# Performance work log

Hardware: AMD Instinct MI355X
Metric: run time of the kernel (lower is better)

Reference implementation:

```python
import jax, jax.numpy as jnp
import numpy as np

B, S, DIN, DH, DOUT = 8, 2048, 512, 1024, 16


def setup_inputs() -> dict:
    key = jax.random.key(0)
    ks = jax.random.split(key, 7)
    x = jax.random.normal(ks[0], (B, S, DIN), dtype=jnp.float32)
    # MLP params (Linear stores W as [in, out] here; we apply x @ W + b)
    w1 = jax.random.normal(ks[1], (DIN, DH), dtype=jnp.float32) / np.sqrt(DIN)
    b1 = jnp.zeros((DH,), dtype=jnp.float32)
    w2 = jax.random.normal(ks[2], (DH, DH), dtype=jnp.float32) / np.sqrt(DH)
    b2 = jnp.zeros((DH,), dtype=jnp.float32)
    w3 = jax.random.normal(ks[3], (DH, DOUT), dtype=jnp.float32) / np.sqrt(DH)
    b3 = jnp.zeros((DOUT,), dtype=jnp.float32)
    # decay buffer: exact dyadics 1 - 2^-(c+3), matches init_kwargs list
    decay = 1.0 - 2.0 ** (-(jnp.arange(DOUT, dtype=jnp.float32) + 3.0))
    # D[i, t, c] = decay_c^(t - i) for t >= i else 0 (upper triangular per channel)
    idx = jnp.arange(S)
    exps = idx[None, :] - idx[:, None]            # [S, S], t - i
    mask = (exps >= 0).astype(jnp.float32)        # triu mask
    exps_c = jnp.maximum(exps, 0).astype(jnp.float32)
    D = mask[:, :, None] * (decay[None, None, :] ** exps_c[:, :, None])  # [S, S, DOUT]
    return {"input_temporal": x, "w1": w1, "b1": b1, "w2": w2, "b2": b2,
            "w3": w3, "b3": b3, "D": D}


def reference(input_temporal, w1, b1, w2, b2, w3, b3, D):
    # 3-layer MLP (dropout=0 -> identity in eval)
    h = jax.nn.relu(input_temporal @ w1 + b1)
    h = jax.nn.relu(h @ w2 + b2)
    o = h @ w3 + b3                               # [B, S, DOUT]
    # decay-weighted causal mixing: out[b,t,c] = sum_{i<=t} o[b,i,c] * decay_c^(t-i)
    # (equivalent to torch repeat+multiply+sum, without materializing [B,S,S,D])
    mixed = jnp.einsum('bic,itc->btc', o, D)
    # extra running cumsum as in the original forward
    return jnp.cumsum(mixed, axis=1)
```

## Files before the change

### kernel.cpp

```cpp
#include <hip/hip_runtime.h>

typedef unsigned int u32;
typedef unsigned short u16;
typedef float f32x4 __attribute__((ext_vector_type(4)));
typedef short bf16x8 __attribute__((ext_vector_type(8)));

__device__ __forceinline__ u16 f2bf(float f) {
  u32 u = __builtin_bit_cast(u32, f);
  u += 0x7FFFu + ((u >> 16) & 1u);
  return (u16)(u >> 16);
}
__device__ __forceinline__ void gload_lds16(const void* g, void* l) {
  __builtin_amdgcn_global_load_lds(
      (const __attribute__((address_space(1))) void*)g,
      (__attribute__((address_space(3))) void*)l, 16, 0, 0);
}

__global__ __launch_bounds__(256) void prep_k(
    const float* __restrict__ x, uint2* __restrict__ A1,
    const float* __restrict__ w1, u16* __restrict__ w1t,
    const float* __restrict__ w2, u16* __restrict__ w2t,
    const float* __restrict__ w3, u16* __restrict__ w3t) {
  const int bid = blockIdx.x;
  const int tid = threadIdx.x;
  if (bid >= 3072) {
    int i = (bid - 3072) * 256 + tid;
    float4 v = ((const float4*)x)[i];
    uint2 o;
    o.x = (u32)f2bf(v.x) | ((u32)f2bf(v.y) << 16);
    o.y = (u32)f2bf(v.z) | ((u32)f2bf(v.w) << 16);
    A1[i] = o;
    return;
  }
  __shared__ float tile[32][33];
  const int z = bid >> 10, t = bid & 1023;
  const int bx = t & 31, by = t >> 5;
  const float* in; u16* out; int R, C;
  if (z == 0)      { in = w1; out = w1t; R = 512;  C = 1024; }
  else if (z == 1) { in = w2; out = w2t; R = 1024; C = 1024; }
  else             { in = w3; out = w3t; R = 1024; C = 16;   }
  int c0 = bx * 32, r0 = by * 32;
  if (c0 >= C || r0 >= R) return;
  int tx = tid & 31, ty = tid >> 5;
  #pragma unroll
  for (int j = 0; j < 4; j++) {
    int r = r0 + ty + j * 8, c = c0 + tx;
    if (r < R && c < C) tile[ty + j * 8][tx] = in[(size_t)r * C + c];
  }
  __syncthreads();
  #pragma unroll
  for (int j = 0; j < 4; j++) {
    int c = c0 + ty + j * 8, r = r0 + tx;
    if (r < R && c < C) out[(size_t)c * R + r] = f2bf(tile[tx][ty + j * 8]);
  }
}

__global__ __launch_bounds__(512, 2) void gemm1p_k(
    const u16* __restrict__ A, const u16* __restrict__ Bt,
    const float* __restrict__ bias, u16* __restrict__ C,
    int M, int N, int K) {
  __shared__ __align__(16) char lds[3 * 49152];
  const int tid = threadIdx.x;
  const int rr = blockIdx.x;
  const int xcd = rr & 7, s_id = rr >> 3;
  const int bm = (xcd << 3) | (s_id >> 2);
  const int bnBase = (s_id & 3) << 1;
  const int wave = tid >> 6, lane = tid & 63;
  const int wm = wave >> 1, wn = wave & 1;
  const int l15 = lane & 15, l4 = lane >> 4;
  const int NT = K >> 6;
  const size_t arow0 = (size_t)bm * 256;

  for (int p = 0; p < 2; p++) {
    const int bn = bnBase + p;
    const size_t brow0 = (size_t)bn * 128;

    f32x4 acc[4][4];
    #pragma unroll
    for (int m = 0; m < 4; m++)
      #pragma unroll
      for (int n = 0; n < 4; n++) acc[m][n] = (f32x4){0.f, 0.f, 0.f, 0.f};

    auto stage = [&](int kt, int s) {
      char* sA = lds + s * 49152;
      char* sB = sA + 32768;
      #pragma unroll
      for (int j = 0; j < 4; j++) {
        int ch = tid + j * 512;
        int row = ch >> 3;
        int col8 = (ch & 7) ^ (row & 7);
        gload_lds16(A + (arow0 + row) * K + kt * 64 + col8 * 8, sA + ch * 16);
      }
      #pragma unroll
      for (int j = 0; j < 2; j++) {
        int ch = tid + j * 512;
        int row = ch >> 3;
        int col8 = (ch & 7) ^ (row & 7);
        gload_lds16(Bt + (brow0 + row) * K + kt * 64 + col8 * 8, sB + ch * 16);
      }
    };

    if (p) __builtin_amdgcn_s_barrier();

    stage(0, 0);
    stage(1, 1);
    asm volatile("s_waitcnt vmcnt(6)" ::: "memory");
    __builtin_amdgcn_s_barrier();

    for (int t = 0; t < NT; t++) {
      const int s = t % 3;
      const char* sA = lds + s * 49152;
      const char* sB = sA + 32768;

      bf16x8 bfr[2][4];
      #pragma unroll
      for (int ks = 0; ks < 2; ks++)
        #pragma unroll
        for (int n = 0; n < 4; n++) {
          int r = wn * 64 + n * 16 + l15;
          bfr[ks][n] = *(const bf16x8*)(sB + r * 128 +
                                        (((ks * 4 + l4) ^ (r & 7)) << 4));
        }
      bf16x8 af0[2][2];
      #pragma unroll
      for (int m = 0; m < 2; m++)
        #pragma unroll
        for (int ks = 0; ks < 2; ks++) {
          int r = wm * 64 + m * 16 + l15;
          af0[m][ks] = *(const bf16x8*)(sA + r * 128 +
                                        (((ks * 4 + l4) ^ (r & 7)) << 4));
        }
      if (t + 2 < NT) stage(t + 2, (t + 2) % 3);

      __builtin_amdgcn_s_barrier();
      asm volatile("s_waitcnt lgkmcnt(0)" ::: "memory");
      __builtin_amdgcn_sched_barrier(0);
      __builtin_amdgcn_s_setprio(1);
      #pragma unroll
      for (int m = 0; m < 2; m++)
        #pragma unroll
        for (int n = 0; n < 4; n++)
          #pragma unroll
          for (int ks = 0; ks < 2; ks++)
            acc[m][n] = __builtin_amdgcn_mfma_f32_16x16x32_bf16(
                af0[m][ks], bfr[ks][n], acc[m][n], 0, 0, 0);
      __builtin_amdgcn_s_setprio(0);

      bf16x8 af1[2][2];
      #pragma unroll
      for (int m = 0; m < 2; m++)
        #pragma unroll
        for (int ks = 0; ks < 2; ks++) {
          int r = wm * 64 + (m + 2) * 16 + l15;
          af1[m][ks] = *(const bf16x8*)(sA + r * 128 +
                                        (((ks * 4 + l4) ^ (r & 7)) << 4));
        }
      __builtin_amdgcn_s_barrier();
      asm volatile("s_waitcnt lgkmcnt(0)" ::: "memory");
      __builtin_amdgcn_sched_barrier(0);
      __builtin_amdgcn_s_setprio(1);
      #pragma unroll
      for (int m = 0; m < 2; m++)
        #pragma unroll
        for (int n = 0; n < 4; n++)
          #pragma unroll
          for (int ks = 0; ks < 2; ks++)
            acc[m + 2][n] = __builtin_amdgcn_mfma_f32_16x16x32_bf16(
                af1[m][ks], bfr[ks][n], acc[m + 2][n], 0, 0, 0);
      __builtin_amdgcn_s_setprio(0);

      if (t + 1 < NT) {
        if (t + 2 < NT)
          asm volatile("s_waitcnt vmcnt(6)" ::: "memory");
        else
          asm volatile("s_waitcnt vmcnt(0)" ::: "memory");
        __builtin_amdgcn_s_barrier();
      }
    }

    #pragma unroll
    for (int n = 0; n < 4; n++) {
      int col = bn * 128 + wn * 64 + n * 16 + l15;
      float bv = bias[col];
      #pragma unroll
      for (int m = 0; m < 4; m++) {
        int row0 = bm * 256 + wm * 64 + m * 16 + l4 * 4;
        #pragma unroll
        for (int r = 0; r < 4; r++) {
          float v = acc[m][n][r] + bv;
          v = v > 0.f ? v : 0.f;
          C[(size_t)(row0 + r) * N + col] = f2bf(v);
        }
      }
    }
  }
}

__global__ __launch_bounds__(512, 2) void gemm2f_k(
    const u16* __restrict__ A, const u16* __restrict__ Bt,
    const float* __restrict__ bias, const u16* __restrict__ w3t,
    float* __restrict__ part, int M, int N, int K) {
  __shared__ __align__(16) char lds[131072];
  const int tid = threadIdx.x;
  const int rr = blockIdx.x;
  const int xcd = rr & 7, slot_id = rr >> 3;
  const int bm = (xcd << 3) | (slot_id >> 2);
  const int bn = slot_id & 3;
  const int wave = tid >> 6, lane = tid & 63;
  const int wm = wave >> 2, wn = wave & 3;
  const int l15 = lane & 15, l4 = lane >> 4;
  const int NT = K >> 5;
  const size_t arow0 = (size_t)bm * 256, brow0 = (size_t)bn * 256;

  f32x4 acc[4][8];
  #pragma unroll
  for (int p = 0; p < 4; p++)
    #pragma unroll
    for (int q = 0; q < 8; q++) acc[p][q] = (f32x4){0.f, 0.f, 0.f, 0.f};

  auto stage = [&](int kt, int s) {
    char* sA = lds + s * 32768;
    char* sB = sA + 16384;
    #pragma unroll
    for (int j = 0; j < 2; j++) {
      int ch = tid + j * 512;
      int row = ch >> 2;
      int col4 = (ch & 3) ^ (row & 3);
      gload_lds16(A + (arow0 + row) * K + kt * 32 + col4 * 8, sA + ch * 16);
    }
    #pragma unroll
    for (int j = 0; j < 2; j++) {
      int ch = tid + j * 512;
      int row = ch >> 2;
      int col4 = (ch & 3) ^ (row & 3);
      gload_lds16(Bt + (brow0 + row) * K + kt * 32 + col4 * 8, sB + ch * 16);
    }
  };

  stage(0, 0);
  stage(1, 1);
  stage(2, 2);
  asm volatile("s_waitcnt vmcnt(8)" ::: "memory");
  __builtin_amdgcn_s_barrier();

  for (int t = 0; t < NT; t++) {
    const int s = t & 3;
    const char* sA = lds + s * 32768;
    const char* sB = sA + 16384;

    bf16x8 bfr[4];
    #pragma unroll
    for (int n = 0; n < 4; n++) {
      int r = wn * 64 + n * 16 + l15;
      bfr[n] = *(const bf16x8*)(sB + r * 64 + ((l4 ^ (r & 3)) << 4));
    }
    bf16x8 af0[4];
    #pragma unroll
    for (int m = 0; m < 4; m++) {
      int r = wm * 128 + m * 16 + l15;
      af0[m] = *(const bf16x8*)(sA + r * 64 + ((l4 ^ (r & 3)) << 4));
    }
    if (t + 3 < NT) stage(t + 3, (t + 3) & 3);

    __builtin_amdgcn_s_barrier();
    asm volatile("s_waitcnt lgkmcnt(0)" ::: "memory");
    __builtin_amdgcn_sched_barrier(0);
    __builtin_amdgcn_s_setprio(1);
    #pragma unroll
    for (int p = 0; p < 4; p++)
      #pragma unroll
      for (int q = 0; q < 4; q++)
        acc[p][q] = __builtin_amdgcn_mfma_f32_16x16x32_bf16(
            bfr[p], af0[q], acc[p][q], 0, 0, 0);
    __builtin_amdgcn_s_setprio(0);

    bf16x8 af1[4];
    #pragma unroll
    for (int m = 0; m < 4; m++) {
      int r = wm * 128 + (m + 4) * 16 + l15;
      af1[m] = *(const bf16x8*)(sA + r * 64 + ((l4 ^ (r & 3)) << 4));
    }
    __builtin_amdgcn_s_barrier();
    asm volatile("s_waitcnt lgkmcnt(0)" ::: "memory");
    __builtin_amdgcn_sched_barrier(0);
    __builtin_amdgcn_s_setprio(1);
    #pragma unroll
    for (int p = 0; p < 4; p++)
      #pragma unroll
      for (int q = 0; q < 4; q++)
        acc[p][q + 4] = __builtin_amdgcn_mfma_f32_16x16x32_bf16(
            bfr[p], af1[q], acc[p][q + 4], 0, 0, 0);
    __builtin_amdgcn_s_setprio(0);

    if (t + 1 < NT) {
      if (t + 3 < NT)
        asm volatile("s_waitcnt vmcnt(8)" ::: "memory");
      else if (t + 2 < NT)
        asm volatile("s_waitcnt vmcnt(4)" ::: "memory");
      else
        asm volatile("s_waitcnt vmcnt(0)" ::: "memory");
      __builtin_amdgcn_s_barrier();
    }
  }

  __builtin_amdgcn_s_barrier();
  #pragma unroll
  for (int p = 0; p < 4; p++) {
    float4 bv = *(const float4*)(bias + wn * 64 + p * 16 + l4 * 4);
    int colb = (wn * 64 + p * 16 + l4 * 4) * 2;
    #pragma unroll
    for (int q = 0; q < 8; q++) {
      int hrow = wm * 128 + q * 16 + l15;
      float v0 = acc[p][q][0] + bv.x; v0 = v0 > 0.f ? v0 : 0.f;
      float v1 = acc[p][q][1] + bv.y; v1 = v1 > 0.f ? v1 : 0.f;
      float v2 = acc[p][q][2] + bv.z; v2 = v2 > 0.f ? v2 : 0.f;
      float v3 = acc[p][q][3] + bv.w; v3 = v3 > 0.f ? v3 : 0.f;
      uint2 pk;
      pk.x = (u32)f2bf(v0) | ((u32)f2bf(v1) << 16);
      pk.y = (u32)f2bf(v2) | ((u32)f2bf(v3) << 16);
      *(uint2*)(lds + hrow * 512 + (colb ^ ((hrow & 7) << 4))) = pk;
    }
  }
  __builtin_amdgcn_s_barrier();

  bf16x8 wf[8];
  {
    const u16* w3row = w3t + (size_t)l15 * 1024 + bn * 256 + l4 * 8;
    #pragma unroll
    for (int kk = 0; kk < 8; kk++)
      wf[kk] = *(const bf16x8*)(w3row + kk * 32);
  }
  #pragma unroll
  for (int g = 0; g < 2; g++) {
    int row0 = wave * 32 + g * 16;
    int row = row0 + l15;
    f32x4 oacc = (f32x4){0.f, 0.f, 0.f, 0.f};
    #pragma unroll
    for (int kk = 0; kk < 8; kk++) {
      bf16x8 hf = *(const bf16x8*)(lds + row * 512 +
                                   ((kk * 64 + l4 * 16) ^ ((row & 7) << 4)));
      oacc = __builtin_amdgcn_mfma_f32_16x16x32_bf16(hf, wf[kk], oacc,
                                                     0, 0, 0);
    }
    int grow = bm * 256 + row0 + l4 * 4;
    int b = grow >> 11, s = grow & 2047;
    float4 st = {oacc[0], oacc[1], oacc[2], oacc[3]};
    *(float4*)(part + ((size_t)bn * 128 + b * 16 + l15) * 2048 + s) = st;
  }
}

__global__ __launch_bounds__(64) void scan_k(
    const float* __restrict__ part, const float* __restrict__ b3,
    float* __restrict__ out) {
  const int chain = blockIdx.x;
  const int lane = threadIdx.x;
  const int b = chain >> 4, c = chain & 15;
  const float dinv = __builtin_bit_cast(float, (u32)((127 - (c + 3)) << 23));
  const float d = 1.f - dinv;
  const float b3c = b3[c];

  float o[32];
  #pragma unroll
  for (int i = 0; i < 8; i++) {
    float4 acc4 = {b3c, b3c, b3c, b3c};
    #pragma unroll
    for (int p = 0; p < 4; p++) {
      const float4* src = (const float4*)(part + (size_t)p * 262144 +
                                          (size_t)chain * 2048 + lane * 32);
      float4 v = src[i];
      acc4.x += v.x; acc4.y += v.y; acc4.z += v.z; acc4.w += v.w;
    }
    o[i * 4 + 0] = acc4.x; o[i * 4 + 1] = acc4.y;
    o[i * 4 + 2] = acc4.z; o[i * 4 + 3] = acc4.w;
  }

  float M = 0.f, A = 0.f, P = 1.f, S = 0.f;
  #pragma unroll
  for (int i = 0; i < 32; i++) {
    M = d * M + o[i];
    A += M;
    P *= d;
    S = d * S + d;
  }

  #pragma unroll
  for (int off = 1; off < 64; off <<= 1) {
    float Pp = __shfl_up(P, off, 64);
    float Mp = __shfl_up(M, off, 64);
    float Sp = __shfl_up(S, off, 64);
    float Ap = __shfl_up(A, off, 64);
    if (lane >= off) {
      float A2 = Ap + S * Mp + A;
      float S2 = Sp + S * Pp;
      float M2 = P * Mp + M;
      float P2 = Pp * P;
      A = A2; S = S2; M = M2; P = P2;
    }
  }
  float m0 = __shfl_up(M, 1, 64);
  float a0 = __shfl_up(A, 1, 64);
  if (lane == 0) { m0 = 0.f; a0 = 0.f; }

  float* dst = out + (size_t)b * 32768 + (size_t)(lane * 32) * 16 + c;
  float m = m0, a = a0;
  #pragma unroll
  for (int i = 0; i < 32; i++) {
    m = d * m + o[i];
    a += m;
    dst[i * 16] = a;
  }
}

extern "C" void kernel_launch(void* const* d_in, const int* in_sizes, int n_in,
                              void* d_out, int out_size, void* d_ws, size_t ws_size,
                              hipStream_t stream) {
  const float* x  = (const float*)d_in[0];
  const float* w1 = (const float*)d_in[1];
  const float* b1 = (const float*)d_in[2];
  const float* w2 = (const float*)d_in[3];
  const float* b2 = (const float*)d_in[4];
  const float* w3 = (const float*)d_in[5];
  const float* b3 = (const float*)d_in[6];
  float* out = (float*)d_out;

  char* ws = (char*)d_ws;
  size_t off = 0;
  u16* A1   = (u16*)(ws + off); off += (size_t)16384 * 512 * 2;
  u16* h1   = (u16*)(ws + off); off += (size_t)16384 * 1024 * 2;
  u16* w1t  = (u16*)(ws + off); off += (size_t)1024 * 512 * 2;
  u16* w2t  = (u16*)(ws + off); off += (size_t)1024 * 1024 * 2;
  u16* w3t  = (u16*)(ws + off); off += (size_t)16 * 1024 * 2;
  float* part = (float*)(ws + off); off += (size_t)4 * 128 * 2048 * 4;

  prep_k<<<11264, 256, 0, stream>>>(x, (uint2*)A1, w1, w1t, w2, w2t, w3, w3t);
  gemm1p_k<<<256, 512, 0, stream>>>(A1, w1t, b1, h1, 16384, 1024, 512);
  gemm2f_k<<<256, 512, 0, stream>>>(h1, w2t, b2, w3t, part,
                                    16384, 1024, 1024);
  scan_k<<<128, 64, 0, stream>>>(part, b3, out);
}
```

Baseline: 84.38 us.

## Compute 256x256 tile in one pass of first GEMM with 4-stage K32 pipeline

The first GEMM kernel used to handle two 128-wide N tiles one after another, reloading the 256-row A tile for each. It now computes a single 256x256 output tile in one K loop, so each A fragment is loaded once and reused against two B halves. The K step drops from 64 to 32 and the LDS ring grows from 3 to 4 stages, with matching swizzle and waitcnt changes. Doubling the accumulators (128 floats per lane) raises register pressure and may hurt occupancy or cause spills at 2 blocks per CU.

```diff
diff --git a/kernel.cpp b/kernel.cpp
--- a/kernel.cpp
+++ b/kernel.cpp
@@ -55,129 +55,118 @@
   }
 }
 
-__global__ __launch_bounds__(512, 2) void gemm1p_k(
+__global__ __launch_bounds__(512, 2) void gemm1d_k(
     const u16* __restrict__ A, const u16* __restrict__ Bt,
     const float* __restrict__ bias, u16* __restrict__ C,
     int M, int N, int K) {
-  __shared__ __align__(16) char lds[3 * 49152];
+  __shared__ __align__(16) char lds[4 * 32768];
   const int tid = threadIdx.x;
   const int rr = blockIdx.x;
-  const int xcd = rr & 7, s_id = rr >> 3;
-  const int bm = (xcd << 3) | (s_id >> 2);
-  const int bnBase = (s_id & 3) << 1;
+  const int xcd = rr & 7, sid = rr >> 3;
+  const int bm = (xcd << 3) | (sid >> 2);
+  const int bnp = sid & 3;
   const int wave = tid >> 6, lane = tid & 63;
   const int wm = wave >> 1, wn = wave & 1;
   const int l15 = lane & 15, l4 = lane >> 4;
-  const int NT = K >> 6;
-  const size_t arow0 = (size_t)bm * 256;
-
-  for (int p = 0; p < 2; p++) {
-    const int bn = bnBase + p;
-    const size_t brow0 = (size_t)bn * 128;
-
-    f32x4 acc[4][4];
+  const int NT = K >> 5;
+  const size_t arow0 = (size_t)bm * 256, brow0 = (size_t)bnp * 256;
+
+  f32x4 acc[2][4][4];
+  #pragma unroll
+  for (int h = 0; h < 2; h++)
     #pragma unroll
     for (int m = 0; m < 4; m++)
       #pragma unroll
-      for (int n = 0; n < 4; n++) acc[m][n] = (f32x4){0.f, 0.f, 0.f, 0.f};
-
-    auto stage = [&](int kt, int s) {
-      char* sA = lds + s * 49152;
-      char* sB = sA + 32768;
-      #pragma unroll
-      for (int j = 0; j < 4; j++) {
-        int ch = tid + j * 512;
-        int row = ch >> 3;
-        int col8 = (ch & 7) ^ (row & 7);
-        gload_lds16(A + (arow0 + row) * K + kt * 64 + col8 * 8, sA + ch * 16);
-      }
-      #pragma unroll
-      for (int j = 0; j < 2; j++) {
-        int ch = tid + j * 512;
-        int row = ch >> 3;
-        int col8 = (ch & 7) ^ (row & 7);
-        gload_lds16(Bt + (brow0 + row) * K + kt * 64 + col8 * 8, sB + ch * 16);
-      }
-    };
-
-    if (p) __builtin_amdgcn_s_barrier();
-
-    stage(0, 0);
-    stage(1, 1);
-    asm volatile("s_waitcnt vmcnt(6)" ::: "memory");
+      for (int n = 0; n < 4; n++) acc[h][m][n] = (f32x4){0.f, 0.f, 0.f, 0.f};
+
+  auto stage = [&](int kt, int s) {
+    char* sA = lds + s * 32768;
+    char* sB = sA + 16384;
+    #pragma unroll
+    for (int j = 0; j < 2; j++) {
+      int ch = tid + j * 512;
+      int row = ch >> 2;
+      int col4 = (ch & 3) ^ (row & 3);
+      gload_lds16(A + (arow0 + row) * K + kt * 32 + col4 * 8, sA + ch * 16);
+    }
+    #pragma unroll
+    for (int j = 0; j < 2; j++) {
+      int ch = tid + j * 512;
+      int row = ch >> 2;
+      int col4 = (ch & 3) ^ (row & 3);
+      gload_lds16(Bt + (brow0 + row) * K + kt * 32 + col4 * 8, sB + ch * 16);
+    }
+  };
+
+  stage(0, 0);
+  stage(1, 1);
+  stage(2, 2);
+  asm volatile("s_waitcnt vmcnt(8)" ::: "memory");
+  __builtin_amdgcn_s_barrier();
+
+  for (int t = 0; t < NT; t++) {
+    const int s = t & 3;
+    const char* sA = lds + s * 32768;
+    const char* sB = sA + 16384;
+
+    bf16x8 af[4];
+    #pragma unroll
+    for (int m = 0; m < 4; m++) {
+      int r = wm * 64 + m * 16 + l15;
+      af[m] = *(const bf16x8*)(sA + r * 64 + ((l4 ^ (r & 3)) << 4));
+    }
+    bf16x8 b0[4];
+    #pragma unroll
+    for (int n = 0; n < 4; n++) {
+      int r = wn * 64 + n * 16 + l15;
+      b0[n] = *(const bf16x8*)(sB + r * 64 + ((l4 ^ (r & 3)) << 4));
+    }
+    if (t + 3 < NT) stage(t + 3, (t + 3) & 3);
+
     __builtin_amdgcn_s_barrier();
-
-    for (int t = 0; t < NT; t++) {
-      const int s = t % 3;
-      const char* sA = lds + s * 49152;
-      const char* sB = sA + 32768;
-
-      bf16x8 bfr[2][4];
-      #pragma unroll
-      for (int ks = 0; ks < 2; ks++)
-        #pragma unroll
-        for (int n = 0; n < 4; n++) {
-          int r = wn * 64 + n * 16 + l15;
-          bfr[ks][n] = *(const bf16x8*)(sB + r * 128 +
-                                        (((ks * 4 + l4) ^ (r & 7)) << 4));
-        }
-      bf16x8 af0[2][2];
-      #pragma unroll
-      for (int m = 0; m < 2; m++)
-        #pragma unroll
-        for (int ks = 0; ks < 2; ks++) {
-          int r = wm * 64 + m * 16 + l15;
-          af0[m][ks] = *(const bf16x8*)(sA + r * 128 +
-                                        (((ks * 4 + l4) ^ (r & 7)) << 4));
-        }
-      if (t + 2 < NT) stage(t + 2, (t + 2) % 3);
-
+    asm volatile("s_waitcnt lgkmcnt(0)" ::: "memory");
+    __builtin_amdgcn_sched_barrier(0);
+    __builtin_amdgcn_s_setprio(1);
+    #pragma unroll
+    for (int m = 0; m < 4; m++)
+      #pragma unroll
+      for (int n = 0; n < 4; n++)
+        acc[0][m][n] = __builtin_amdgcn_mfma_f32_16x16x32_bf16(
+            af[m], b0[n], acc[0][m][n], 0, 0, 0);
+    __builtin_amdgcn_s_setprio(0);
+
+    bf16x8 b1[4];
+    #pragma unroll
+    for (int n = 0; n < 4; n++) {
+      int r = 128 + wn * 64 + n * 16 + l15;
+      b1[n] = *(const bf16x8*)(sB + r * 64 + ((l4 ^ (r & 3)) << 4));
+    }
+    __builtin_amdgcn_s_barrier();
+    asm volatile("s_waitcnt lgkmcnt(0)" ::: "memory");
+    __builtin_amdgcn_sched_barrier(0);
+    __builtin_amdgcn_s_setprio(1);
+    #pragma unroll
+    for (int m = 0; m < 4; m++)
+      #pragma unroll
+      for (int n = 0; n < 4; n++)
+        acc[1][m][n] = __builtin_amdgcn_mfma_f32_16x16x32_bf16(
+            af[m], b1[n], acc[1][m][n], 0, 0, 0);
+    __builtin_amdgcn_s_setprio(0);
+
+    if (t + 1 < NT) {
+      if (t + 3 < NT)
+        asm volatile("s_waitcnt vmcnt(8)" ::: "memory");
+      else if (t + 2 < NT)
+        asm volatile("s_waitcnt vmcnt(4)" ::: "memory");
+      else
+        asm volatile("s_waitcnt vmcnt(0)" ::: "memory");
       __builtin_amdgcn_s_barrier();
-      asm volatile("s_waitcnt lgkmcnt(0)" ::: "memory");
-      __builtin_amdgcn_sched_barrier(0);
-      __builtin_amdgcn_s_setprio(1);
-      #pragma unroll
-      for (int m = 0; m < 2; m++)
-        #pragma unroll
-        for (int n = 0; n < 4; n++)
-          #pragma unroll
-          for (int ks = 0; ks < 2; ks++)
-            acc[m][n] = __builtin_amdgcn_mfma_f32_16x16x32_bf16(
-                af0[m][ks], bfr[ks][n], acc[m][n], 0, 0, 0);
-      __builtin_amdgcn_s_setprio(0);
-
-      bf16x8 af1[2][2];
-      #pragma unroll
-      for (int m = 0; m < 2; m++)
-        #pragma unroll
-        for (int ks = 0; ks < 2; ks++) {
-          int r = wm * 64 + (m + 2) * 16 + l15;
-          af1[m][ks] = *(const bf16x8*)(sA + r * 128 +
-                                        (((ks * 4 + l4) ^ (r & 7)) << 4));
-        }
-      __builtin_amdgcn_s_barrier();
-      asm volatile("s_waitcnt lgkmcnt(0)" ::: "memory");
-      __builtin_amdgcn_sched_barrier(0);
-      __builtin_amdgcn_s_setprio(1);
-      #pragma unroll
-      for (int m = 0; m < 2; m++)
-        #pragma unroll
-        for (int n = 0; n < 4; n++)
-          #pragma unroll
-          for (int ks = 0; ks < 2; ks++)
-            acc[m + 2][n] = __builtin_amdgcn_mfma_f32_16x16x32_bf16(
-                af1[m][ks], bfr[ks][n], acc[m + 2][n], 0, 0, 0);
-      __builtin_amdgcn_s_setprio(0);
-
-      if (t + 1 < NT) {
-        if (t + 2 < NT)
-          asm volatile("s_waitcnt vmcnt(6)" ::: "memory");
-        else
-          asm volatile("s_waitcnt vmcnt(0)" ::: "memory");
-        __builtin_amdgcn_s_barrier();
-      }
-    }
-
+    }
+  }
+
+  #pragma unroll
+  for (int h = 0; h < 2; h++) {
+    int bn = bnp * 2 + h;
     #pragma unroll
     for (int n = 0; n < 4; n++) {
       int col = bn * 128 + wn * 64 + n * 16 + l15;
@@ -187,7 +176,7 @@
         int row0 = bm * 256 + wm * 64 + m * 16 + l4 * 4;
         #pragma unroll
         for (int r = 0; r < 4; r++) {
-          float v = acc[m][n][r] + bv;
+          float v = acc[h][m][n][r] + bv;
           v = v > 0.f ? v : 0.f;
           C[(size_t)(row0 + r) * N + col] = f2bf(v);
         }
@@ -433,7 +422,7 @@
   float* part = (float*)(ws + off); off += (size_t)4 * 128 * 2048 * 4;
 
   prep_k<<<11264, 256, 0, stream>>>(x, (uint2*)A1, w1, w1t, w2, w2t, w3, w3t);
-  gemm1p_k<<<256, 512, 0, stream>>>(A1, w1t, b1, h1, 16384, 1024, 512);
+  gemm1d_k<<<256, 512, 0, stream>>>(A1, w1t, b1, h1, 16384, 1024, 512);
   gemm2f_k<<<256, 512, 0, stream>>>(h1, w2t, b2, w3t, part,
                                     16384, 1024, 1024);
   scan_k<<<128, 64, 0, stream>>>(part, b3, out);
```

New measurement: 82.00 us. 2.8% less time.
